# Kernel optimization log

Hardware: AMD Instinct MI355X
Metric: run time of the kernel (lower is better)

Reference implementation:

```python
import jax, jax.numpy as jnp
import numpy as np

B, S, H, E = 8, 2048, 1024, 8
CAP_FACTOR = 1.25  # deepspeed-style capacity factor for top-1 gating


def setup_inputs() -> dict:
    key = jax.random.key(0)
    ks = jax.random.split(key, 10)
    sc = 0.02
    return {
        "x": jax.random.normal(ks[0], (B, S, H), jnp.float32),
        "W_in": jax.random.normal(ks[1], (H, H), jnp.float32) * sc,
        "b_in": jnp.zeros((H,), jnp.float32),
        "W_gate": jax.random.normal(ks[2], (H, E), jnp.float32) * sc,
        "W1": jax.random.normal(ks[3], (E, H, H), jnp.float32) * sc,
        "b1": jnp.zeros((E, H), jnp.float32),
        "W2": jax.random.normal(ks[4], (E, H, H), jnp.float32) * sc,
        "b2": jnp.zeros((E, H), jnp.float32),
        "Wr1": jax.random.normal(ks[5], (H, H), jnp.float32) * sc,
        "br1": jnp.zeros((H,), jnp.float32),
        "Wr2": jax.random.normal(ks[6], (H, H), jnp.float32) * sc,
        "br2": jnp.zeros((H,), jnp.float32),
        "W_coef": jax.random.normal(ks[7], (H, 2), jnp.float32) * sc,
        "b_coef": jnp.zeros((2,), jnp.float32),
        "W_out": jax.random.normal(ks[8], (H, H), jnp.float32) * sc,
        "b_out": jnp.zeros((H,), jnp.float32),
    }


def _moe(x, W_gate, W1, b1, W2, b2, Wr1, br1, Wr2, br2, W_coef, b_coef):
    # x: [T, H] flattened tokens. Top-1 gating with capacity dropping + residual expert.
    T, Hd = x.shape
    nE = W_gate.shape[1]
    cap = int(np.ceil(CAP_FACTOR * T / nE))  # static under jit

    gates = jax.nn.softmax(x @ W_gate)                  # [T, E]
    eidx = jnp.argmax(gates, axis=-1)                    # [T]
    mask1 = jax.nn.one_hot(eidx, nE, dtype=x.dtype)      # [T, E]
    pos = jnp.cumsum(mask1, axis=0) - 1.0                # position within each expert
    pos_tok = jnp.take_along_axis(pos, eidx[:, None], 1)[:, 0].astype(jnp.int32)
    keep = (pos_tok < cap).astype(x.dtype)               # capacity drop mask
    gate_val = jnp.take_along_axis(gates, eidx[:, None], 1)[:, 0] * keep  # [T]
    slot = jnp.minimum(pos_tok, cap - 1)                 # safe slot index

    # scatter tokens into [E, cap, H] buffers (dropped tokens contribute zeros)
    disp = jnp.zeros((nE, cap, Hd), x.dtype).at[eidx, slot].add(x * keep[:, None])
    h = jax.nn.relu(jnp.einsum('ech,ehf->ecf', disp, W1) + b1[:, None, :])
    eo = jnp.einsum('ecf,efg->ecg', h, W2) + b2[:, None, :]
    moe_out = eo[eidx, slot] * gate_val[:, None]         # gather back; dropped -> 0

    # residual expert on all tokens, mixed with learned 2-way softmax coefficient
    res = jax.nn.relu(x @ Wr1 + br1) @ Wr2 + br2
    coef = jax.nn.softmax(x @ W_coef + b_coef)           # [T, 2]
    return moe_out * coef[:, :1] + res * coef[:, 1:]


def reference(x, W_in, b_in, W_gate, W1, b1, W2, b2, Wr1, br1, Wr2, br2,
              W_coef, b_coef, W_out, b_out):
    Bb, Ss, Hd = x.shape
    t = x.reshape(-1, Hd) @ W_in + b_in
    t = _moe(t, W_gate, W1, b1, W2, b2, Wr1, br1, Wr2, br2, W_coef, b_coef)
    t = t @ W_out + b_out
    return t.reshape(Bb, Ss, Hd)
```

## Files before the change

kernel.cpp:

```cpp
#include <hip/hip_runtime.h>
#include <cstdint>

#define T_TOK 16384
#define HD    1024
#define NE    8
#define CAP   2560
#define NCHUNK (T_TOK / 64)

typedef __attribute__((ext_vector_type(4))) float f32x4;
typedef __attribute__((ext_vector_type(8))) short bf16x8;

__device__ __forceinline__ unsigned short f2bf(float f) {
    union { float f; unsigned u; } x{f};
    unsigned r = x.u + 0x7FFF + ((x.u >> 16) & 1);
    return (unsigned short)(r >> 16);
}

__device__ __forceinline__ void gload_lds16(const unsigned short* g, unsigned short* l) {
    __builtin_amdgcn_global_load_lds(
        (const __attribute__((address_space(1))) void*)g,
        (__attribute__((address_space(3))) void*)l, 16, 0, 0);
}

template<bool GATHER, bool RELU, bool ROWSCALE, bool SCATTER, bool OUTBF16>
__global__ __launch_bounds__(512)
void gemm_bf16_k(const unsigned short* __restrict__ A,
                 const unsigned short* __restrict__ Bt,
                 const float* __restrict__ bias,
                 void* __restrict__ Cv,
                 int M, int N, int K,
                 const int* __restrict__ idxTab,
                 const float* __restrict__ rs,
                 const float* __restrict__ addsrc,
                 long aB, long bB, long biasB, long tabB, long cB)
{
    const int nx = gridDim.x, ny = gridDim.y;
    long nwg = (long)nx * ny * gridDim.z;
    long flat = blockIdx.x + (long)nx * (blockIdx.y + (long)ny * blockIdx.z);
    long cpx = nwg >> 3;
    long swz = (flat & 7) * cpx + (flat >> 3);
    const int bx = (int)(swz % nx);
    const int by = (int)((swz / nx) % ny);
    const int bz = (int)(swz / ((long)nx * ny));

    A  += (long)bz * aB;
    Bt += (long)bz * bB;
    const float* bptr = bias + (long)bz * biasB;
    const int* tab = idxTab ? idxTab + (long)bz * tabB : nullptr;
    float*          Cf = (float*)Cv + (long)bz * cB;
    unsigned short* Cb = (unsigned short*)Cv + (long)bz * cB;

    __shared__ unsigned short As[256][64];
    __shared__ unsigned short Bs[128][64];

    const int tid  = threadIdx.x;
    const int wv   = tid >> 6;
    const int lane = tid & 63;
    const int m0 = by * 256, n0 = bx * 128;

    const int srow = lane >> 3;
    const int schk = lane & 7;

    const unsigned short* aSrc[4];
    const unsigned short* bSrc[2];
    #pragma unroll
    for (int i = 0; i < 4; ++i) {
        int lrow = wv * 32 + i * 8 + srow;
        int scol = ((schk ^ (lrow & 7)) * 8);
        long sr;
        if (GATHER) { int tr = tab[m0 + lrow]; sr = tr < 0 ? 0 : tr; }
        else        sr = m0 + lrow;
        aSrc[i] = A + sr * (long)K + scol;
    }
    #pragma unroll
    for (int i = 0; i < 2; ++i) {
        int lrow = wv * 16 + i * 8 + srow;
        int scol = ((schk ^ (lrow & 7)) * 8);
        bSrc[i] = Bt + (long)(n0 + lrow) * K + scol;
    }

    f32x4 acc[4][4] = {};
    const int wm = wv >> 1, wn = wv & 1;
    const int fr = lane & 15, kg = lane >> 4;

    for (int k0 = 0; k0 < K; k0 += 64) {
        __syncthreads();
        #pragma unroll
        for (int i = 0; i < 4; ++i)
            gload_lds16(aSrc[i] + k0, &As[wv * 32 + i * 8][0]);
        #pragma unroll
        for (int i = 0; i < 2; ++i)
            gload_lds16(bSrc[i] + k0, &Bs[wv * 16 + i * 8][0]);
        __syncthreads();

        #pragma unroll
        for (int kk = 0; kk < 2; ++kk) {
            bf16x8 af[4], bfr[4];
            #pragma unroll
            for (int i2 = 0; i2 < 4; ++i2) {
                int R = wm * 64 + i2 * 16 + fr;
                af[i2] = *(const bf16x8*)&As[R][((kk * 4 + kg) ^ (R & 7)) * 8];
            }
            #pragma unroll
            for (int j2 = 0; j2 < 4; ++j2) {
                int R = wn * 64 + j2 * 16 + fr;
                bfr[j2] = *(const bf16x8*)&Bs[R][((kk * 4 + kg) ^ (R & 7)) * 8];
            }
            #pragma unroll
            for (int i2 = 0; i2 < 4; ++i2)
                #pragma unroll
                for (int j2 = 0; j2 < 4; ++j2)
                    acc[i2][j2] = __builtin_amdgcn_mfma_f32_16x16x32_bf16(
                        af[i2], bfr[j2], acc[i2][j2], 0, 0, 0);
        }
    }

    const int colL = lane & 15, rgrp = (lane >> 4) * 4;
    #pragma unroll
    for (int i2 = 0; i2 < 4; ++i2) {
        #pragma unroll
        for (int r = 0; r < 4; ++r) {
            int gm = m0 + wm * 64 + i2 * 16 + rgrp + r;
            int token = gm; float sc = 1.0f;
            if (SCATTER) {
                token = tab[gm];
                if (token < 0) continue;
                sc = rs[token];
            } else if (ROWSCALE) {
                sc = rs[gm];
            }
            #pragma unroll
            for (int j2 = 0; j2 < 4; ++j2) {
                int gn = n0 + wn * 64 + j2 * 16 + colL;
                float v = acc[i2][j2][r] + bptr[gn];
                if (RELU) v = fmaxf(v, 0.0f);
                if (SCATTER) {
                    long idx = (long)token * N + gn;
                    if (OUTBF16) Cb[idx] = f2bf(addsrc[idx] + v * sc);
                    else         Cf[idx] += v * sc;
                } else {
                    if (ROWSCALE) v *= sc;
                    if (OUTBF16) Cb[(long)gm * N + gn] = f2bf(v);
                    else         Cf[(long)gm * N + gn] = v;
                }
            }
        }
    }
}

__global__ __launch_bounds__(256)
void drop_cast_k(const float* __restrict__ mix, unsigned short* __restrict__ mixb,
                 const int* __restrict__ droplist, const int* __restrict__ dropcnt)
{
    const int cnt = *dropcnt;
    for (int i = blockIdx.x; i < cnt; i += gridDim.x) {
        const int tok = droplist[i];
        const float4* src = (const float4*)(mix + (long)tok * HD);
        ushort4* dst = (ushort4*)(mixb + (long)tok * HD);
        const int j = threadIdx.x;
        float4 v = src[j];
        ushort4 o;
        o.x = f2bf(v.x); o.y = f2bf(v.y); o.z = f2bf(v.z); o.w = f2bf(v.w);
        dst[j] = o;
    }
}

__global__ __launch_bounds__(256)
void transpose_cast_k(const float* __restrict__ W, unsigned short* __restrict__ Wt,
                      int K, int N, long wB, long wtB)
{
    const int z = blockIdx.z;
    W  += (long)z * wB;
    Wt += (long)z * wtB;
    __shared__ float tile[64][65];
    const int k0 = blockIdx.x * 64, n0 = blockIdx.y * 64;
    const int c = threadIdx.x & 63, r4 = threadIdx.x >> 6;
    #pragma unroll 4
    for (int it = 0; it < 16; ++it) {
        int row = it * 4 + r4;
        tile[row][c] = W[(long)(k0 + row) * N + n0 + c];
    }
    __syncthreads();
    #pragma unroll 4
    for (int it = 0; it < 16; ++it) {
        int nrow = it * 4 + r4;
        Wt[(long)(n0 + nrow) * K + k0 + c] = f2bf(tile[c][nrow]);
    }
}

__global__ __launch_bounds__(256)
void wsmall_k(const float* __restrict__ W_in, const float* __restrict__ W_gate,
              const float* __restrict__ W_coef,
              float* __restrict__ wgp, float* __restrict__ wcp)
{
    const int r = blockIdx.x * 4 + (threadIdx.x >> 6);
    const int lane = threadIdx.x & 63;
    float s[10] = {};
    for (int k = lane; k < HD; k += 64) {
        float a = W_in[(long)r * HD + k];
        const float4* g = (const float4*)(W_gate + (long)k * 8);
        float4 g0 = g[0], g1 = g[1];
        s[0] += a * g0.x; s[1] += a * g0.y; s[2] += a * g0.z; s[3] += a * g0.w;
        s[4] += a * g1.x; s[5] += a * g1.y; s[6] += a * g1.z; s[7] += a * g1.w;
        float2 cv = *(const float2*)(W_coef + (long)k * 2);
        s[8] += a * cv.x; s[9] += a * cv.y;
    }
    #pragma unroll
    for (int off = 32; off > 0; off >>= 1)
        #pragma unroll
        for (int e = 0; e < 10; ++e) s[e] += __shfl_xor(s[e], off);
    if (lane == 0) {
        #pragma unroll
        for (int e = 0; e < 8; ++e) wgp[(long)r * 8 + e] = s[e];
        wcp[(long)r * 2 + 0] = s[8];
        wcp[(long)r * 2 + 1] = s[9];
    }
}

__global__ void gbias_k(const float* __restrict__ b_in, const float* __restrict__ W_gate,
                        const float* __restrict__ W_coef, const float* __restrict__ b_coef,
                        float* __restrict__ bg, float* __restrict__ bc)
{
    const int lane = threadIdx.x;
    float s[10] = {};
    for (int k = lane; k < HD; k += 64) {
        float a = b_in[k];
        const float4* g = (const float4*)(W_gate + (long)k * 8);
        float4 g0 = g[0], g1 = g[1];
        s[0] += a * g0.x; s[1] += a * g0.y; s[2] += a * g0.z; s[3] += a * g0.w;
        s[4] += a * g1.x; s[5] += a * g1.y; s[6] += a * g1.z; s[7] += a * g1.w;
        float2 cv = *(const float2*)(W_coef + (long)k * 2);
        s[8] += a * cv.x; s[9] += a * cv.y;
    }
    #pragma unroll
    for (int off = 32; off > 0; off >>= 1)
        #pragma unroll
        for (int e = 0; e < 10; ++e) s[e] += __shfl_xor(s[e], off);
    if (lane == 0) {
        #pragma unroll
        for (int e = 0; e < 8; ++e) bg[e] = s[e];
        bc[0] = s[8] + b_coef[0];
        bc[1] = s[9] + b_coef[1];
    }
}

__global__ __launch_bounds__(256)
void gating_k(const float* __restrict__ x,
              const float* __restrict__ Wg,
              const float* __restrict__ Wc,
              const float* __restrict__ bg,
              const float* __restrict__ bc,
              unsigned short* __restrict__ xb,
              int* __restrict__ eidx,
              float* __restrict__ gval,
              float* __restrict__ coef0,
              float* __restrict__ coef1)
{
    const int tok = (blockIdx.x * 256 + threadIdx.x) >> 6;
    const int lane = threadIdx.x & 63;
    const float* row = x + (long)tok * HD;
    unsigned short* orow = xb + (long)tok * HD;

    float acc[8] = {};
    float c0 = 0.f, c1 = 0.f;
    for (int i = 0; i < HD / 64; ++i) {
        int k = i * 64 + lane;
        float tv = row[k];
        orow[k] = f2bf(tv);
        const float4* wg = (const float4*)(Wg + (long)k * 8);
        float4 w0 = wg[0], w1 = wg[1];
        acc[0] = fmaf(tv, w0.x, acc[0]); acc[1] = fmaf(tv, w0.y, acc[1]);
        acc[2] = fmaf(tv, w0.z, acc[2]); acc[3] = fmaf(tv, w0.w, acc[3]);
        acc[4] = fmaf(tv, w1.x, acc[4]); acc[5] = fmaf(tv, w1.y, acc[5]);
        acc[6] = fmaf(tv, w1.z, acc[6]); acc[7] = fmaf(tv, w1.w, acc[7]);
        float2 wcv = *(const float2*)(Wc + (long)k * 2);
        c0 = fmaf(tv, wcv.x, c0);
        c1 = fmaf(tv, wcv.y, c1);
    }
    #pragma unroll
    for (int off = 32; off > 0; off >>= 1) {
        #pragma unroll
        for (int e = 0; e < 8; ++e) acc[e] += __shfl_xor(acc[e], off);
        c0 += __shfl_xor(c0, off);
        c1 += __shfl_xor(c1, off);
    }
    if (lane == 0) {
        #pragma unroll
        for (int e = 0; e < 8; ++e) acc[e] += bg[e];
        float m = acc[0]; int best = 0;
        #pragma unroll
        for (int e = 1; e < 8; ++e) if (acc[e] > m) { m = acc[e]; best = e; }
        float s = 0.f;
        #pragma unroll
        for (int e = 0; e < 8; ++e) s += expf(acc[e] - m);
        eidx[tok] = best;
        gval[tok] = 1.0f / s;
        float l0 = c0 + bc[0], l1 = c1 + bc[1];
        float mm = fmaxf(l0, l1);
        float e0 = expf(l0 - mm), e1 = expf(l1 - mm);
        float inv = 1.0f / (e0 + e1);
        coef0[tok] = e0 * inv;
        coef1[tok] = e1 * inv;
    }
}

__global__ void scan_hist_k(const int* __restrict__ eidx,
                            int* __restrict__ counts,
                            int* __restrict__ idxTab)
{
    const int b = blockIdx.x;
    const int lane = threadIdx.x;
    for (int j = b * 64 + lane; j < NE * CAP; j += NCHUNK * 64)
        idxTab[j] = -1;
    int e = eidx[b * 64 + lane];
    #pragma unroll
    for (int ex = 0; ex < NE; ++ex) {
        unsigned long long msk = __ballot(e == ex);
        if (lane == ex) counts[b * NE + ex] = (int)__popcll(msk);
    }
}

__global__ void scan_offsets_k(const int* __restrict__ counts,
                               int* __restrict__ offsets,
                               int* __restrict__ dropcnt)
{
    const int e = threadIdx.x;
    if (e == 63) *dropcnt = 0;
    if (e < NE) {
        int run = 0;
        for (int b = 0; b < NCHUNK; ++b) {
            offsets[b * NE + e] = run;
            run += counts[b * NE + e];
        }
    }
}

__global__ void scan_fill_k(const int* __restrict__ eidx,
                            const float* __restrict__ gval,
                            const float* __restrict__ coef0,
                            const int* __restrict__ offsets,
                            int* __restrict__ idxTab,
                            float* __restrict__ smoe,
                            int* __restrict__ droplist,
                            int* __restrict__ dropcnt)
{
    const int b = blockIdx.x;
    const int lane = threadIdx.x;
    const int tok = b * 64 + lane;
    int e = eidx[tok];
    unsigned long long below = (lane == 0) ? 0ull : ((~0ull) >> (64 - lane));
    int myrank = 0;
    #pragma unroll
    for (int ex = 0; ex < NE; ++ex) {
        unsigned long long msk = __ballot(e == ex);
        if (e == ex) myrank = (int)__popcll(msk & below) + offsets[b * NE + ex];
    }
    if (myrank < CAP) {
        idxTab[e * CAP + myrank] = tok;
        smoe[tok] = gval[tok] * coef0[tok];
    } else {
        smoe[tok] = 0.0f;
        int di = atomicAdd(dropcnt, 1);
        droplist[di] = tok;
    }
}

extern "C" void kernel_launch(void* const* d_in, const int* in_sizes, int n_in,
                              void* d_out, int out_size, void* d_ws, size_t ws_size,
                              hipStream_t stream)
{
    const float* x      = (const float*)d_in[0];
    const float* W_in   = (const float*)d_in[1];
    const float* b_in   = (const float*)d_in[2];
    const float* W_gate = (const float*)d_in[3];
    const float* W1     = (const float*)d_in[4];
    const float* b1     = (const float*)d_in[5];
    const float* W2     = (const float*)d_in[6];
    const float* b2     = (const float*)d_in[7];
    const float* Wr1    = (const float*)d_in[8];
    const float* br1    = (const float*)d_in[9];
    const float* Wr2    = (const float*)d_in[10];
    const float* br2    = (const float*)d_in[11];
    const float* W_coef = (const float*)d_in[12];
    const float* b_coef = (const float*)d_in[13];
    const float* W_out  = (const float*)d_in[14];
    const float* b_out  = (const float*)d_in[15];
    float* out = (float*)d_out;

    const size_t MiB = 1024 * 1024;
    char* ws = (char*)d_ws;
    unsigned short* W1T  = (unsigned short*)(ws + 0);
    unsigned short* res1 = (unsigned short*)(ws + 0);
    unsigned short* mixb = (unsigned short*)(ws + 0);
    unsigned short* h    = (unsigned short*)(ws + 32 * MiB);
    unsigned short* t_b  = (unsigned short*)(ws + 72 * MiB);
    unsigned short* W2T  = (unsigned short*)(ws + 104 * MiB);
    unsigned short* WinT = (unsigned short*)(ws + 120 * MiB);
    unsigned short* Wr1T = (unsigned short*)(ws + 122 * MiB);
    unsigned short* Wr2T = (unsigned short*)(ws + 124 * MiB);
    unsigned short* WoutT= (unsigned short*)(ws + 126 * MiB);
    char* sm = ws + 128 * MiB;
    float* wgp  = (float*)(sm);            sm += HD * 8 * 4;
    float* wcp  = (float*)(sm);            sm += HD * 2 * 4;
    float* bg   = (float*)(sm);            sm += 64;
    float* bc   = (float*)(sm);            sm += 64;
    int*   eidx = (int*)(sm);              sm += T_TOK * 4;
    float* gval = (float*)(sm);            sm += T_TOK * 4;
    float* cf0  = (float*)(sm);            sm += T_TOK * 4;
    float* cf1  = (float*)(sm);            sm += T_TOK * 4;
    float* smoe = (float*)(sm);            sm += T_TOK * 4;
    int* idxTab = (int*)(sm);              sm += NE * CAP * 4;
    int* counts = (int*)(sm);              sm += NCHUNK * NE * 4;
    int* offs   = (int*)(sm);              sm += NCHUNK * NE * 4;
    int* droplist = (int*)(sm);            sm += T_TOK * 4;
    int* dropcnt  = (int*)(sm);            sm += 64;
    unsigned short* xb = (unsigned short*)d_out;
    float* mix = out;
    (void)ws_size; (void)in_sizes; (void)n_in; (void)out_size;

    dim3 blk(256);
    dim3 blkG(512);
    dim3 gT(16, 16, 1);
    dim3 gT8(16, 16, 8);
    dim3 gBig(HD / 128, T_TOK / 256, 1);
    dim3 gExp(HD / 128, CAP / 256, NE);

    transpose_cast_k<<<gT,  blk, 0, stream>>>(W_in,  WinT,  HD, HD, 0, 0);
    transpose_cast_k<<<gT,  blk, 0, stream>>>(Wr1,   Wr1T,  HD, HD, 0, 0);
    transpose_cast_k<<<gT,  blk, 0, stream>>>(Wr2,   Wr2T,  HD, HD, 0, 0);
    transpose_cast_k<<<gT,  blk, 0, stream>>>(W_out, WoutT, HD, HD, 0, 0);
    transpose_cast_k<<<gT8, blk, 0, stream>>>(W1, W1T, HD, HD, (long)HD * HD, (long)HD * HD);
    transpose_cast_k<<<gT8, blk, 0, stream>>>(W2, W2T, HD, HD, (long)HD * HD, (long)HD * HD);
    wsmall_k<<<HD / 4, blk, 0, stream>>>(W_in, W_gate, W_coef, wgp, wcp);
    gbias_k<<<1, 64, 0, stream>>>(b_in, W_gate, W_coef, b_coef, bg, bc);
    gating_k<<<T_TOK / 4, blk, 0, stream>>>(x, wgp, wcp, bg, bc, xb,
                                            eidx, gval, cf0, cf1);
    scan_hist_k<<<NCHUNK, 64, 0, stream>>>(eidx, counts, idxTab);
    scan_offsets_k<<<1, 64, 0, stream>>>(counts, offs, dropcnt);
    scan_fill_k<<<NCHUNK, 64, 0, stream>>>(eidx, gval, cf0, offs, idxTab, smoe,
                                           droplist, dropcnt);
    gemm_bf16_k<false, false, false, false, true><<<gBig, blkG, 0, stream>>>(
        xb, WinT, b_in, t_b, T_TOK, HD, HD, nullptr, nullptr, nullptr,
        0, 0, 0, 0, 0);
    gemm_bf16_k<true, true, false, false, true><<<gExp, blkG, 0, stream>>>(
        t_b, W1T, b1, h, CAP, HD, HD, idxTab, nullptr, nullptr,
        0, (long)HD * HD, HD, CAP, (long)CAP * HD);
    gemm_bf16_k<false, true, false, false, true><<<gBig, blkG, 0, stream>>>(
        t_b, Wr1T, br1, res1, T_TOK, HD, HD, nullptr, nullptr, nullptr,
        0, 0, 0, 0, 0);
    gemm_bf16_k<false, false, true, false, false><<<gBig, blkG, 0, stream>>>(
        res1, Wr2T, br2, mix, T_TOK, HD, HD, nullptr, cf1, nullptr,
        0, 0, 0, 0, 0);
    gemm_bf16_k<false, false, false, true, true><<<gExp, blkG, 0, stream>>>(
        h, W2T, b2, mixb, CAP, HD, HD, idxTab, smoe, mix,
        (long)CAP * HD, (long)HD * HD, HD, CAP, 0);
    drop_cast_k<<<256, blk, 0, stream>>>(mix, mixb, droplist, dropcnt);
    gemm_bf16_k<false, false, false, false, false><<<gBig, blkG, 0, stream>>>(
        mixb, WoutT, b_out, out, T_TOK, HD, HD, nullptr, nullptr, nullptr,
        0, 0, 0, 0, 0);
}
```

Baseline: 405.3 us.

## Triple-buffer LDS tiles and interleave async loads with MFMA phases

```diff
diff --git a/kernel.cpp b/kernel.cpp
--- a/kernel.cpp
+++ b/kernel.cpp
@@ -20,6 +20,32 @@
     __builtin_amdgcn_global_load_lds(
         (const __attribute__((address_space(1))) void*)g,
         (__attribute__((address_space(3))) void*)l, 16, 0, 0);
+}
+
+__device__ __forceinline__ void phase_mfma(
+    const unsigned short (&A)[256][64], const unsigned short (&B)[128][64],
+    f32x4 (&acc)[4][4], int wm, int wn, int fr, int kg, int kk)
+{
+    bf16x8 af[4], bfr[4];
+    #pragma unroll
+    for (int i2 = 0; i2 < 4; ++i2) {
+        int R = wm * 64 + i2 * 16 + fr;
+        af[i2] = *(const bf16x8*)&A[R][((kk * 4 + kg) ^ (R & 7)) * 8];
+    }
+    #pragma unroll
+    for (int j2 = 0; j2 < 4; ++j2) {
+        int R = wn * 64 + j2 * 16 + fr;
+        bfr[j2] = *(const bf16x8*)&B[R][((kk * 4 + kg) ^ (R & 7)) * 8];
+    }
+    __builtin_amdgcn_s_barrier();
+    __builtin_amdgcn_s_setprio(1);
+    #pragma unroll
+    for (int i2 = 0; i2 < 4; ++i2)
+        #pragma unroll
+        for (int j2 = 0; j2 < 4; ++j2)
+            acc[i2][j2] = __builtin_amdgcn_mfma_f32_16x16x32_bf16(
+                af[i2], bfr[j2], acc[i2][j2], 0, 0, 0);
+    __builtin_amdgcn_s_setprio(0);
 }
 
 template<bool GATHER, bool RELU, bool ROWSCALE, bool SCATTER, bool OUTBF16>
@@ -50,19 +76,23 @@
     float*          Cf = (float*)Cv + (long)bz * cB;
     unsigned short* Cb = (unsigned short*)Cv + (long)bz * cB;
 
-    __shared__ unsigned short As[256][64];
-    __shared__ unsigned short Bs[128][64];
+    const int m0 = by * 256, n0 = bx * 128;
+
+    if ((GATHER || SCATTER) && tab[m0] < 0) return;
+
+    __shared__ unsigned short As[3][256][64];
+    __shared__ unsigned short Bs[3][128][64];
 
     const int tid  = threadIdx.x;
     const int wv   = tid >> 6;
     const int lane = tid & 63;
-    const int m0 = by * 256, n0 = bx * 128;
 
     const int srow = lane >> 3;
     const int schk = lane & 7;
 
     const unsigned short* aSrc[4];
     const unsigned short* bSrc[2];
+    int aRow[4], bRow[2];
     #pragma unroll
     for (int i = 0; i < 4; ++i) {
         int lrow = wv * 32 + i * 8 + srow;
@@ -71,48 +101,61 @@
         if (GATHER) { int tr = tab[m0 + lrow]; sr = tr < 0 ? 0 : tr; }
         else        sr = m0 + lrow;
         aSrc[i] = A + sr * (long)K + scol;
+        aRow[i] = wv * 32 + i * 8;
     }
     #pragma unroll
     for (int i = 0; i < 2; ++i) {
         int lrow = wv * 16 + i * 8 + srow;
         int scol = ((schk ^ (lrow & 7)) * 8);
         bSrc[i] = Bt + (long)(n0 + lrow) * K + scol;
+        bRow[i] = wv * 16 + i * 8;
     }
 
     f32x4 acc[4][4] = {};
     const int wm = wv >> 1, wn = wv & 1;
     const int fr = lane & 15, kg = lane >> 4;
-
-    for (int k0 = 0; k0 < K; k0 += 64) {
-        __syncthreads();
-        #pragma unroll
-        for (int i = 0; i < 4; ++i)
-            gload_lds16(aSrc[i] + k0, &As[wv * 32 + i * 8][0]);
-        #pragma unroll
-        for (int i = 0; i < 2; ++i)
-            gload_lds16(bSrc[i] + k0, &Bs[wv * 16 + i * 8][0]);
-        __syncthreads();
-
-        #pragma unroll
-        for (int kk = 0; kk < 2; ++kk) {
-            bf16x8 af[4], bfr[4];
-            #pragma unroll
-            for (int i2 = 0; i2 < 4; ++i2) {
-                int R = wm * 64 + i2 * 16 + fr;
-                af[i2] = *(const bf16x8*)&As[R][((kk * 4 + kg) ^ (R & 7)) * 8];
-            }
-            #pragma unroll
-            for (int j2 = 0; j2 < 4; ++j2) {
-                int R = wn * 64 + j2 * 16 + fr;
-                bfr[j2] = *(const bf16x8*)&Bs[R][((kk * 4 + kg) ^ (R & 7)) * 8];
-            }
-            #pragma unroll
-            for (int i2 = 0; i2 < 4; ++i2)
-                #pragma unroll
-                for (int j2 = 0; j2 < 4; ++j2)
-                    acc[i2][j2] = __builtin_amdgcn_mfma_f32_16x16x32_bf16(
-                        af[i2], bfr[j2], acc[i2][j2], 0, 0, 0);
+    const int NT = K >> 6;
+
+    #pragma unroll
+    for (int i = 0; i < 4; ++i) gload_lds16(aSrc[i],      &As[0][aRow[i]][0]);
+    #pragma unroll
+    for (int i = 0; i < 2; ++i) gload_lds16(bSrc[i],      &Bs[0][bRow[i]][0]);
+    #pragma unroll
+    for (int i = 0; i < 4; ++i) gload_lds16(aSrc[i] + 64, &As[1][aRow[i]][0]);
+    #pragma unroll
+    for (int i = 0; i < 2; ++i) gload_lds16(bSrc[i] + 64, &Bs[1][bRow[i]][0]);
+    asm volatile("s_waitcnt vmcnt(6)" ::: "memory");
+    __builtin_amdgcn_s_barrier();
+
+    for (int t = 0; t < NT - 1; ++t) {
+        const int rb = t % 3;
+        const int sb = (t + 2) % 3;
+        const bool doStage = (t + 2) < NT;
+        const int k0s = (t + 2) << 6;
+
+        if (doStage) {
+            gload_lds16(aSrc[0] + k0s, &As[sb][aRow[0]][0]);
+            gload_lds16(aSrc[1] + k0s, &As[sb][aRow[1]][0]);
+            gload_lds16(bSrc[0] + k0s, &Bs[sb][bRow[0]][0]);
         }
+        phase_mfma(As[rb], Bs[rb], acc, wm, wn, fr, kg, 0);
+        __builtin_amdgcn_s_barrier();
+
+        if (doStage) {
+            gload_lds16(aSrc[2] + k0s, &As[sb][aRow[2]][0]);
+            gload_lds16(aSrc[3] + k0s, &As[sb][aRow[3]][0]);
+            gload_lds16(bSrc[1] + k0s, &Bs[sb][bRow[1]][0]);
+        }
+        phase_mfma(As[rb], Bs[rb], acc, wm, wn, fr, kg, 1);
+        if (t == NT - 2) asm volatile("s_waitcnt vmcnt(0)" ::: "memory");
+        else             asm volatile("s_waitcnt vmcnt(6)" ::: "memory");
+        __builtin_amdgcn_s_barrier();
+    }
+    {
+        const int rb = (NT - 1) % 3;
+        phase_mfma(As[rb], Bs[rb], acc, wm, wn, fr, kg, 0);
+        __builtin_amdgcn_s_barrier();
+        phase_mfma(As[rb], Bs[rb], acc, wm, wn, fr, kg, 1);
     }
 
     const int colL = lane & 15, rgrp = (lane >> 4) * 4;
```

Result: slower. 576.5 us (+42.2%).
